# Kernel tuning notes

Measured on AMD Instinct MI355X. Metric: run time of the kernel, lower is better.

Reference implementation:

```python
import jax, jax.numpy as jnp
import numpy as np

NEVENT = 1024
NSTEP = 64
NWINDOW = 2048
NHID = 128
NLAYER = 2


def _lstm_layer(x, Wih, Whh, bih, bhh):
    # x: [B, T, D]; PyTorch gate order: i, f, g, o
    B = x.shape[0]
    H = Whh.shape[1]
    h0 = jnp.zeros((B, H), x.dtype)
    c0 = jnp.zeros((B, H), x.dtype)
    b = bih + bhh

    def step(carry, xt):
        h, c = carry
        gates = xt @ Wih.T + h @ Whh.T + b  # [B, 4H]
        i, f, g, o = jnp.split(gates, 4, axis=-1)
        i = jax.nn.sigmoid(i)
        f = jax.nn.sigmoid(f)
        g = jnp.tanh(g)
        o = jax.nn.sigmoid(o)
        c = f * c + i * g
        h = o * jnp.tanh(c)
        return (h, c), h

    _, ys = jax.lax.scan(step, (h0, c0), jnp.swapaxes(x, 0, 1))  # ys: [T, B, H]
    return jnp.swapaxes(ys, 0, 1)


def _lstm(x, layers):
    for p in layers:
        x = _lstm_layer(x, *p)
    return x


def setup_inputs() -> dict:
    key = jax.random.key(0)
    ks = jax.random.split(key, 32)
    bound = 1.0 / np.sqrt(NHID)

    def u(k, shape):
        return jax.random.uniform(k, shape, jnp.float32, -bound, bound)

    inp = {"sequential": jax.random.randint(ks[0], (NWINDOW, NSTEP), 0, NEVENT)}
    i = 1
    for name, in0 in [("seq", 1), ("quant", NEVENT)]:
        for l in range(NLAYER):
            d = in0 if l == 0 else NHID
            inp[f"{name}_Wih{l}"] = u(ks[i], (4 * NHID, d)); i += 1
            inp[f"{name}_Whh{l}"] = u(ks[i], (4 * NHID, NHID)); i += 1
            inp[f"{name}_bih{l}"] = u(ks[i], (4 * NHID,)); i += 1
            inp[f"{name}_bhh{l}"] = u(ks[i], (4 * NHID,)); i += 1
    inp["cls_W"] = u(ks[i], (NEVENT, 2 * NHID)); i += 1
    inp["cls_b"] = u(ks[i], (NEVENT,))
    return inp


def reference(sequential,
              seq_Wih0, seq_Whh0, seq_bih0, seq_bhh0,
              seq_Wih1, seq_Whh1, seq_bih1, seq_bhh1,
              quant_Wih0, quant_Whh0, quant_bih0, quant_bhh0,
              quant_Wih1, quant_Whh1, quant_bih1, quant_bhh1,
              cls_W, cls_b):
    # sequential branch: embed (nemb=1 -> unsqueeze) then 2-layer LSTM
    seq_x = sequential[:, :, None].astype(jnp.float32)  # [B, T, 1]
    seq_out = _lstm(seq_x, [(seq_Wih0, seq_Whh0, seq_bih0, seq_bhh0),
                            (seq_Wih1, seq_Whh1, seq_bih1, seq_bhh1)])

    # quantitative branch: cumulative event-count histogram per window
    # (vectorized equivalent of the nested Counter loops): one-hot + cumsum over time
    quant = jnp.cumsum(jax.nn.one_hot(sequential, NEVENT, dtype=jnp.float32), axis=1)  # [B, T, E]
    quant_out = _lstm(quant, [(quant_Wih0, quant_Whh0, quant_bih0, quant_bhh0),
                              (quant_Wih1, quant_Whh1, quant_bih1, quant_bhh1)])

    out = jnp.concatenate([seq_out[:, -1], quant_out[:, -1]], axis=1)  # [B, 2H]
    return out @ cls_W.T + cls_b  # [B, nevent]
```

## Files before the change

kernel.cpp:

```cpp
#include <hip/hip_runtime.h>
#include <hip/hip_bf16.h>
#include <math.h>

#define NEVENT 1024
#define NSTEP 64
#define NWINDOW 2048
#define NHID 128
#define NG 512
#define WPB 8

typedef __attribute__((ext_vector_type(8))) short bf16x8;
typedef __attribute__((ext_vector_type(4))) float f32x4;

__device__ __forceinline__ unsigned short f2bf(float f){
  unsigned int u = __float_as_uint(f);
  return (unsigned short)((u + 0x7FFFu + ((u >> 16) & 1u)) >> 16);
}
__device__ __forceinline__ float sigm(float x){
  return __builtin_amdgcn_rcpf(1.0f + __expf(-x));
}
__device__ __forceinline__ float tanh_f(float x){
  float e = __expf(2.0f * x);
  return 1.0f - 2.0f * __builtin_amdgcn_rcpf(e + 1.0f);
}
__device__ __forceinline__ void lgkm_barrier(){
  asm volatile("s_waitcnt lgkmcnt(0)" ::: "memory");
  __builtin_amdgcn_s_barrier();
}
#define SWZ(row, byte) ((byte) ^ (((row) & 7) << 4))

__global__ void transpose_k(const float* __restrict__ in, float* __restrict__ out, int R, int C){
  int idx = blockIdx.x*256 + threadIdx.x;
  if (idx < R*C){ int r = idx / C, c = idx - r*C; out[c*R + r] = in[idx]; }
}

__global__ void pack6_k(const float* __restrict__ s0, const float* __restrict__ s1,
                        const float* __restrict__ s2, const float* __restrict__ s3,
                        const float* __restrict__ s4, const float* __restrict__ s5,
                        unsigned short* __restrict__ dst){
  int g = blockIdx.x >> 5;
  int i = (blockIdx.x & 31)*256 + threadIdx.x;
  const float* src = (g==0)?s0:(g==1)?s1:(g==2)?s2:(g==3)?s3:(g==4)?s4:s5;
  unsigned short* d = dst + g*65536;
  int lane = i & 63; int n = (i >> 6) & 31; int kt = i >> 11;
  int col = 16*n + (lane & 15);
  int k0  = 32*kt + 8*(lane >> 4);
  #pragma unroll
  for (int j = 0; j < 8; ++j)
    d[i*8 + j] = f2bf(src[col*128 + k0 + j]);
}

__global__ __launch_bounds__(512, 2)
void lstm_fused_k(const int* __restrict__ seqtok,
    const float* __restrict__ sWih0,
    const float* __restrict__ sb0i, const float* __restrict__ sb0h,
    const float* __restrict__ sb1i, const float* __restrict__ sb1h,
    const float* __restrict__ qb0i, const float* __restrict__ qb0h,
    const float* __restrict__ qb1i, const float* __restrict__ qb1h,
    const unsigned short* __restrict__ pWhh0_s, const unsigned short* __restrict__ pWih1_s,
    const unsigned short* __restrict__ pWhh1_s,
    const unsigned short* __restrict__ pWhh0_q, const unsigned short* __restrict__ pWih1_q,
    const unsigned short* __restrict__ pWhh1_q,
    const float* __restrict__ qWqT,
    float* __restrict__ hseq, float* __restrict__ hq)
{
  __shared__ uint4 wih1[8192];
  __shared__ __attribute__((aligned(16))) unsigned short h0buf[2][2048];
  __shared__ __attribute__((aligned(16))) unsigned short h1buf[2][2048];
  __shared__ int sAll[16*64];

  const int tid  = threadIdx.x;
  const int lane = tid & 63;
  const int nw   = tid >> 6;
  const bool quant = (blockIdx.x >= 128);
  const int blk  = quant ? (int)blockIdx.x - 128 : (int)blockIdx.x;
  const int w0   = blk * 16;

  const uint4* wsrc = (const uint4*)(quant ? pWih1_q : pWih1_s);
  for (int i = tid; i < 8192; i += 512) wih1[i] = wsrc[i];
  for (int i = tid; i < 16*64; i += 512){ int w = i >> 6, t = i & 63; sAll[i] = seqtok[(w0 + w)*64 + t]; }
  for (int i = tid; i < 2048; i += 512){ h0buf[0][i] = 0; h1buf[0][i] = 0; }

  const int jcol  = 16*nw + (lane & 15);
  const int rbase = 4*(lane >> 4);
  const float* b0i = quant ? qb0i : sb0i; const float* b0h = quant ? qb0h : sb0h;
  const float* b1i = quant ? qb1i : sb1i; const float* b1h = quant ? qb1h : sb1h;
  float b0c[4], b1c[4], wc[4];
  #pragma unroll
  for (int q = 0; q < 4; ++q){
    int col = 128*q + jcol;
    b0c[q] = b0i[col] + b0h[col];
    b1c[q] = b1i[col] + b1h[col];
    wc[q]  = sWih0[col];
  }

  const unsigned short* p0 = quant ? pWhh0_q : pWhh0_s;
  const unsigned short* p1 = quant ? pWhh1_q : pWhh1_s;
  bf16x8 whh0f[4][4], whh1f[4][4];
  #pragma unroll
  for (int q = 0; q < 4; ++q)
    #pragma unroll
    for (int kt = 0; kt < 4; ++kt){
      int idx = ((kt*32 + 8*q + nw)*64 + lane)*8;
      whh0f[q][kt] = *(const bf16x8*)(p0 + idx);
      whh1f[q][kt] = *(const bf16x8*)(p1 + idx);
    }

  float zr[4][4], pref[4][4];
  float c0[4] = {0,0,0,0}, c1[4] = {0,0,0,0};
  #pragma unroll
  for (int q = 0; q < 4; ++q)
    #pragma unroll
    for (int r = 0; r < 4; ++r){ zr[q][r] = b0c[q]; pref[q][r] = 0.0f; }

  char* const h0base = (char*)h0buf;
  char* const h1base = (char*)h1buf;
  float* const houtp = quant ? hq : hseq;

  __syncthreads();

  {
    float g0[4][4];
    if (quant){
      #pragma unroll
      for (int r = 0; r < 4; ++r){
        int s = sAll[(rbase + r)*64 + 0];
        #pragma unroll
        for (int q = 0; q < 4; ++q) pref[q][r] = qWqT[s*512 + 128*q + jcol];
      }
      #pragma unroll
      for (int q = 0; q < 4; ++q)
        #pragma unroll
        for (int r = 0; r < 4; ++r){ zr[q][r] += pref[q][r]; g0[q][r] = zr[q][r]; }
      #pragma unroll
      for (int r = 0; r < 4; ++r){
        int s = sAll[(rbase + r)*64 + 1];
        #pragma unroll
        for (int q = 0; q < 4; ++q) pref[q][r] = qWqT[s*512 + 128*q + jcol];
      }
    } else {
      #pragma unroll
      for (int r = 0; r < 4; ++r){
        float sv = (float)sAll[(rbase + r)*64 + 0];
        #pragma unroll
        for (int q = 0; q < 4; ++q) g0[q][r] = fmaf(sv, wc[q], b0c[q]);
      }
    }
    #pragma unroll
    for (int r = 0; r < 4; ++r){
      float iv = sigm(g0[0][r]);
      float gv = tanh_f(g0[2][r]);
      float ov = sigm(g0[3][r]);
      c0[r] = iv * gv;
      float h = ov * tanh_f(c0[r]);
      int row = rbase + r;
      *(unsigned short*)(h0base + 4096 + SWZ(row, row*256 + jcol*2)) = f2bf(h);
    }
  }
  __syncthreads();

  for (int t = 0; t < NSTEP-1; ++t){
    char* h0rd = h0base + ((t+1)&1)*4096;
    char* h1rd = h1base + ((t  )&1)*4096;
    char* h0wr = h0base + ((t  )&1)*4096;
    char* h1wr = h1base + ((t+1)&1)*4096;

    {
      f32x4 acc[4];
      #pragma unroll
      for (int q = 0; q < 4; ++q){ f32x4 a; a[0]=b1c[q]; a[1]=b1c[q]; a[2]=b1c[q]; a[3]=b1c[q]; acc[q] = a; }
      #pragma unroll
      for (int kt = 0; kt < 4; ++kt){
        int row = lane & 15;
        int off = SWZ(row, row*256 + kt*64 + (lane>>4)*16);
        const bf16x8 a0 = *(const bf16x8*)(h0rd + off);
        const bf16x8 a1 = *(const bf16x8*)(h1rd + off);
        #pragma unroll
        for (int q = 0; q < 4; ++q){
          const bf16x8 wi = *(const bf16x8*)((const char*)wih1 + ((kt*32 + 8*q + nw)*64 + lane)*16);
          acc[q] = __builtin_amdgcn_mfma_f32_16x16x32_bf16(a0, wi,           acc[q], 0, 0, 0);
          acc[q] = __builtin_amdgcn_mfma_f32_16x16x32_bf16(a1, whh1f[q][kt], acc[q], 0, 0, 0);
        }
      }
      #pragma unroll
      for (int r = 0; r < 4; ++r){
        float iv = sigm(acc[0][r]), fv = sigm(acc[1][r]);
        float gv = tanh_f(acc[2][r]), ov = sigm(acc[3][r]);
        c1[r] = fv*c1[r] + iv*gv;
        float h = ov * tanh_f(c1[r]);
        int row = rbase + r;
        *(unsigned short*)(h1wr + SWZ(row, row*256 + jcol*2)) = f2bf(h);
      }
    }

    {
      f32x4 acc[4];
      if (quant){
        #pragma unroll
        for (int q = 0; q < 4; ++q){
          f32x4 a;
          #pragma unroll
          for (int r = 0; r < 4; ++r){ zr[q][r] += pref[q][r]; a[r] = zr[q][r]; }
          acc[q] = a;
        }
        if (t < NSTEP-2){
          #pragma unroll
          for (int r = 0; r < 4; ++r){
            int s = sAll[(rbase + r)*64 + t + 2];
            #pragma unroll
            for (int q = 0; q < 4; ++q) pref[q][r] = qWqT[s*512 + 128*q + jcol];
          }
        }
      } else {
        float sv[4];
        #pragma unroll
        for (int r = 0; r < 4; ++r) sv[r] = (float)sAll[(rbase + r)*64 + t + 1];
        #pragma unroll
        for (int q = 0; q < 4; ++q){
          f32x4 a;
          #pragma unroll
          for (int r = 0; r < 4; ++r) a[r] = fmaf(sv[r], wc[q], b0c[q]);
          acc[q] = a;
        }
      }
      #pragma unroll
      for (int kt = 0; kt < 4; ++kt){
        int row = lane & 15;
        int off = SWZ(row, row*256 + kt*64 + (lane>>4)*16);
        const bf16x8 a0 = *(const bf16x8*)(h0rd + off);
        #pragma unroll
        for (int q = 0; q < 4; ++q)
          acc[q] = __builtin_amdgcn_mfma_f32_16x16x32_bf16(a0, whh0f[q][kt], acc[q], 0, 0, 0);
      }
      #pragma unroll
      for (int r = 0; r < 4; ++r){
        float iv = sigm(acc[0][r]), fv = sigm(acc[1][r]);
        float gv = tanh_f(acc[2][r]), ov = sigm(acc[3][r]);
        c0[r] = fv*c0[r] + iv*gv;
        float h = ov * tanh_f(c0[r]);
        int row = rbase + r;
        *(unsigned short*)(h0wr + SWZ(row, row*256 + jcol*2)) = f2bf(h);
      }
    }

    lgkm_barrier();
  }

  {
    const int t = NSTEP-1;
    char* h0rd = h0base + ((t+1)&1)*4096;
    char* h1rd = h1base + ((t  )&1)*4096;
    f32x4 acc[4];
    #pragma unroll
    for (int q = 0; q < 4; ++q){ f32x4 a; a[0]=b1c[q]; a[1]=b1c[q]; a[2]=b1c[q]; a[3]=b1c[q]; acc[q] = a; }
    #pragma unroll
    for (int kt = 0; kt < 4; ++kt){
      int row = lane & 15;
      int off = SWZ(row, row*256 + kt*64 + (lane>>4)*16);
      const bf16x8 a0 = *(const bf16x8*)(h0rd + off);
      const bf16x8 a1 = *(const bf16x8*)(h1rd + off);
      #pragma unroll
      for (int q = 0; q < 4; ++q){
        const bf16x8 wi = *(const bf16x8*)((const char*)wih1 + ((kt*32 + 8*q + nw)*64 + lane)*16);
        acc[q] = __builtin_amdgcn_mfma_f32_16x16x32_bf16(a0, wi,           acc[q], 0, 0, 0);
        acc[q] = __builtin_amdgcn_mfma_f32_16x16x32_bf16(a1, whh1f[q][kt], acc[q], 0, 0, 0);
      }
    }
    #pragma unroll
    for (int r = 0; r < 4; ++r){
      float iv = sigm(acc[0][r]), fv = sigm(acc[1][r]);
      float gv = tanh_f(acc[2][r]), ov = sigm(acc[3][r]);
      c1[r] = fv*c1[r] + iv*gv;
      float h = ov * tanh_f(c1[r]);
      int row = rbase + r;
      houtp[(w0 + row)*128 + jcol] = h;
    }
  }
}

__global__ __launch_bounds__(256, 4)
void cls_k(const float* __restrict__ hseq, const float* __restrict__ hq,
           const float* __restrict__ clsWT, const float* __restrict__ clsb,
           float* __restrict__ out)
{
  __shared__ float hcat[WPB][2*NHID];
  const int tid = threadIdx.x;
  const int w0 = blockIdx.x * WPB;
  for (int i = tid; i < WPB*2*NHID; i += 256){
    int w = i >> 8; int j = i & (2*NHID-1);
    hcat[w][j] = (j < NHID) ? hseq[(w0+w)*NHID + j] : hq[(w0+w)*NHID + (j - NHID)];
  }
  __syncthreads();
  float acc[4][WPB];
  #pragma unroll
  for (int p=0;p<4;++p)
    #pragma unroll
    for (int w=0;w<WPB;++w) acc[p][w] = 0.0f;
  for (int j = 0; j < 2*NHID; ++j){
    float wv0 = clsWT[j*NEVENT + tid];
    float wv1 = clsWT[j*NEVENT + tid + 256];
    float wv2 = clsWT[j*NEVENT + tid + 512];
    float wv3 = clsWT[j*NEVENT + tid + 768];
    #pragma unroll
    for (int w=0; w<WPB; ++w){
      float hv = hcat[w][j];
      acc[0][w] = fmaf(hv, wv0, acc[0][w]);
      acc[1][w] = fmaf(hv, wv1, acc[1][w]);
      acc[2][w] = fmaf(hv, wv2, acc[2][w]);
      acc[3][w] = fmaf(hv, wv3, acc[3][w]);
    }
  }
  #pragma unroll
  for (int p=0;p<4;++p){
    float bb = clsb[tid + p*256];
    #pragma unroll
    for (int w=0;w<WPB;++w)
      out[(w0+w)*NEVENT + tid + p*256] = acc[p][w] + bb;
  }
}

extern "C" void kernel_launch(void* const* d_in, const int* in_sizes, int n_in,
                              void* d_out, int out_size, void* d_ws, size_t ws_size,
                              hipStream_t stream) {
  const int*   seqtok = (const int*)  d_in[0];
  const float* sWih0  = (const float*)d_in[1];
  const float* sWhh0  = (const float*)d_in[2];
  const float* sb0i   = (const float*)d_in[3];
  const float* sb0h   = (const float*)d_in[4];
  const float* sWih1  = (const float*)d_in[5];
  const float* sWhh1  = (const float*)d_in[6];
  const float* sb1i   = (const float*)d_in[7];
  const float* sb1h   = (const float*)d_in[8];
  const float* qWih0  = (const float*)d_in[9];
  const float* qWhh0  = (const float*)d_in[10];
  const float* qb0i   = (const float*)d_in[11];
  const float* qb0h   = (const float*)d_in[12];
  const float* qWih1  = (const float*)d_in[13];
  const float* qWhh1  = (const float*)d_in[14];
  const float* qb1i   = (const float*)d_in[15];
  const float* qb1h   = (const float*)d_in[16];
  const float* clsW   = (const float*)d_in[17];
  const float* clsb   = (const float*)d_in[18];

  float* ws = (float*)d_ws;
  float* qWqT  = ws;
  float* clsWT = ws + 524288;
  float* hseq  = ws + 786432;
  float* hq    = ws + 1048576;
  unsigned short* pk = (unsigned short*)(ws + 1310720);
  unsigned short* pWhh0_s = pk;
  unsigned short* pWih1_s = pk + 65536;
  unsigned short* pWhh1_s = pk + 131072;
  unsigned short* pWhh0_q = pk + 196608;
  unsigned short* pWih1_q = pk + 262144;
  unsigned short* pWhh1_q = pk + 327680;

  transpose_k<<<(NG*NEVENT + 255)/256, 256, 0, stream>>>(qWih0, qWqT, NG, NEVENT);
  transpose_k<<<(NEVENT*2*NHID + 255)/256, 256, 0, stream>>>(clsW, clsWT, NEVENT, 2*NHID);
  pack6_k<<<192, 256, 0, stream>>>(sWhh0, sWih1, sWhh1, qWhh0, qWih1, qWhh1, pk);

  lstm_fused_k<<<256, 512, 0, stream>>>(seqtok, sWih0,
      sb0i, sb0h, sb1i, sb1h, qb0i, qb0h, qb1i, qb1h,
      pWhh0_s, pWih1_s, pWhh1_s, pWhh0_q, pWih1_q, pWhh1_q,
      qWqT, hseq, hq);

  cls_k<<<NWINDOW/WPB, 256, 0, stream>>>(hseq, hq, clsWT, clsb, (float*)d_out);
}
```

Baseline: 224.5 us.

## Fuse prep kernels with tiled transpose and hold Wih1 fragments in registers

Merges the two transpose launches and the pack kernel into one prep kernel, and replaces the naive strided transpose with a 32x32 shared-memory tiled transpose so both reads and writes are coalesced. In the LSTM kernel, the layer-1 input weights move from a 128KB shared-memory array into per-thread register fragments, which removes their LDS reads each step and frees LDS. The layer-0 step also reuses the h0 fragments already loaded for layer 1 instead of reading them from LDS again. The cost is 64 more VGPRs per thread for the extra fragments, under launch bounds of 512 threads and 2 blocks, so register spills or lower occupancy are possible.

Measured after the change: 485.5 us. 2.16x slower.

```diff
diff --git a/kernel.cpp b/kernel.cpp
--- a/kernel.cpp
+++ b/kernel.cpp
@@ -29,25 +29,47 @@
 }
 #define SWZ(row, byte) ((byte) ^ (((row) & 7) << 4))
 
-__global__ void transpose_k(const float* __restrict__ in, float* __restrict__ out, int R, int C){
-  int idx = blockIdx.x*256 + threadIdx.x;
-  if (idx < R*C){ int r = idx / C, c = idx - r*C; out[c*R + r] = in[idx]; }
-}
-
-__global__ void pack6_k(const float* __restrict__ s0, const float* __restrict__ s1,
-                        const float* __restrict__ s2, const float* __restrict__ s3,
-                        const float* __restrict__ s4, const float* __restrict__ s5,
-                        unsigned short* __restrict__ dst){
-  int g = blockIdx.x >> 5;
-  int i = (blockIdx.x & 31)*256 + threadIdx.x;
-  const float* src = (g==0)?s0:(g==1)?s1:(g==2)?s2:(g==3)?s3:(g==4)?s4:s5;
-  unsigned short* d = dst + g*65536;
-  int lane = i & 63; int n = (i >> 6) & 31; int kt = i >> 11;
-  int col = 16*n + (lane & 15);
-  int k0  = 32*kt + 8*(lane >> 4);
-  #pragma unroll
-  for (int j = 0; j < 8; ++j)
-    d[i*8 + j] = f2bf(src[col*128 + k0 + j]);
+__global__ __launch_bounds__(256)
+void prep_k(const float* __restrict__ qWih0, float* __restrict__ qWqT,
+            const float* __restrict__ clsW,  float* __restrict__ clsWT,
+            const float* __restrict__ s0, const float* __restrict__ s1,
+            const float* __restrict__ s2, const float* __restrict__ s3,
+            const float* __restrict__ s4, const float* __restrict__ s5,
+            unsigned short* __restrict__ dst)
+{
+  const int b = blockIdx.x;
+  if (b < 768){
+    const float* in; float* out; int R, C, bb;
+    if (b < 512){ in = qWih0; out = qWqT; R = NG;     C = NEVENT; bb = b; }
+    else        { in = clsW;  out = clsWT; R = NEVENT; C = 2*NHID; bb = b - 512; }
+    __shared__ float tl[32][33];
+    const int nbx = C >> 5;
+    const int by = bb / nbx, bx = bb - by*nbx;
+    const int tx = threadIdx.x & 31, ty = threadIdx.x >> 5;
+    #pragma unroll
+    for (int k = 0; k < 4; ++k){
+      int r = by*32 + ty + k*8;
+      tl[ty + k*8][tx] = in[r*C + bx*32 + tx];
+    }
+    __syncthreads();
+    #pragma unroll
+    for (int k = 0; k < 4; ++k){
+      int r = bx*32 + ty + k*8;
+      out[r*R + by*32 + tx] = tl[tx][ty + k*8];
+    }
+  } else {
+    const int bb = b - 768;
+    const int g = bb >> 5;
+    const int i = (bb & 31)*256 + threadIdx.x;
+    const float* src = (g==0)?s0:(g==1)?s1:(g==2)?s2:(g==3)?s3:(g==4)?s4:s5;
+    unsigned short* d = dst + g*65536;
+    const int lane = i & 63; const int n = (i >> 6) & 31; const int kt = i >> 11;
+    const int col = 16*n + (lane & 15);
+    const int k0  = 32*kt + 8*(lane >> 4);
+    #pragma unroll
+    for (int j = 0; j < 8; ++j)
+      d[i*8 + j] = f2bf(src[col*128 + k0 + j]);
+  }
 }
 
 __global__ __launch_bounds__(512, 2)
@@ -64,7 +86,6 @@
     const float* __restrict__ qWqT,
     float* __restrict__ hseq, float* __restrict__ hq)
 {
-  __shared__ uint4 wih1[8192];
   __shared__ __attribute__((aligned(16))) unsigned short h0buf[2][2048];
   __shared__ __attribute__((aligned(16))) unsigned short h1buf[2][2048];
   __shared__ int sAll[16*64];
@@ -76,8 +97,6 @@
   const int blk  = quant ? (int)blockIdx.x - 128 : (int)blockIdx.x;
   const int w0   = blk * 16;
 
-  const uint4* wsrc = (const uint4*)(quant ? pWih1_q : pWih1_s);
-  for (int i = tid; i < 8192; i += 512) wih1[i] = wsrc[i];
   for (int i = tid; i < 16*64; i += 512){ int w = i >> 6, t = i & 63; sAll[i] = seqtok[(w0 + w)*64 + t]; }
   for (int i = tid; i < 2048; i += 512){ h0buf[0][i] = 0; h1buf[0][i] = 0; }
 
@@ -96,7 +115,8 @@
 
   const unsigned short* p0 = quant ? pWhh0_q : pWhh0_s;
   const unsigned short* p1 = quant ? pWhh1_q : pWhh1_s;
-  bf16x8 whh0f[4][4], whh1f[4][4];
+  const unsigned short* pw = quant ? pWih1_q : pWih1_s;
+  bf16x8 whh0f[4][4], whh1f[4][4], wih1f[4][4];
   #pragma unroll
   for (int q = 0; q < 4; ++q)
     #pragma unroll
@@ -104,6 +124,7 @@
       int idx = ((kt*32 + 8*q + nw)*64 + lane)*8;
       whh0f[q][kt] = *(const bf16x8*)(p0 + idx);
       whh1f[q][kt] = *(const bf16x8*)(p1 + idx);
+      wih1f[q][kt] = *(const bf16x8*)(pw + idx);
     }
 
   float zr[4][4], pref[4][4];
@@ -165,6 +186,8 @@
     char* h0wr = h0base + ((t  )&1)*4096;
     char* h1wr = h1base + ((t+1)&1)*4096;
 
+    bf16x8 a0f[4];
+
     {
       f32x4 acc[4];
       #pragma unroll
@@ -175,10 +198,10 @@
         int off = SWZ(row, row*256 + kt*64 + (lane>>4)*16);
         const bf16x8 a0 = *(const bf16x8*)(h0rd + off);
         const bf16x8 a1 = *(const bf16x8*)(h1rd + off);
+        a0f[kt] = a0;
         #pragma unroll
         for (int q = 0; q < 4; ++q){
-          const bf16x8 wi = *(const bf16x8*)((const char*)wih1 + ((kt*32 + 8*q + nw)*64 + lane)*16);
-          acc[q] = __builtin_amdgcn_mfma_f32_16x16x32_bf16(a0, wi,           acc[q], 0, 0, 0);
+          acc[q] = __builtin_amdgcn_mfma_f32_16x16x32_bf16(a0, wih1f[q][kt], acc[q], 0, 0, 0);
           acc[q] = __builtin_amdgcn_mfma_f32_16x16x32_bf16(a1, whh1f[q][kt], acc[q], 0, 0, 0);
         }
       }
@@ -224,14 +247,10 @@
         }
       }
       #pragma unroll
-      for (int kt = 0; kt < 4; ++kt){
-        int row = lane & 15;
-        int off = SWZ(row, row*256 + kt*64 + (lane>>4)*16);
-        const bf16x8 a0 = *(const bf16x8*)(h0rd + off);
+      for (int kt = 0; kt < 4; ++kt)
         #pragma unroll
         for (int q = 0; q < 4; ++q)
-          acc[q] = __builtin_amdgcn_mfma_f32_16x16x32_bf16(a0, whh0f[q][kt], acc[q], 0, 0, 0);
-      }
+          acc[q] = __builtin_amdgcn_mfma_f32_16x16x32_bf16(a0f[kt], whh0f[q][kt], acc[q], 0, 0, 0);
       #pragma unroll
       for (int r = 0; r < 4; ++r){
         float iv = sigm(acc[0][r]), fv = sigm(acc[1][r]);
@@ -261,8 +280,7 @@
       const bf16x8 a1 = *(const bf16x8*)(h1rd + off);
       #pragma unroll
       for (int q = 0; q < 4; ++q){
-        const bf16x8 wi = *(const bf16x8*)((const char*)wih1 + ((kt*32 + 8*q + nw)*64 + lane)*16);
-        acc[q] = __builtin_amdgcn_mfma_f32_16x16x32_bf16(a0, wi,           acc[q], 0, 0, 0);
+        acc[q] = __builtin_amdgcn_mfma_f32_16x16x32_bf16(a0, wih1f[q][kt], acc[q], 0, 0, 0);
         acc[q] = __builtin_amdgcn_mfma_f32_16x16x32_bf16(a1, whh1f[q][kt], acc[q], 0, 0, 0);
       }
     }
@@ -355,9 +373,8 @@
   unsigned short* pWih1_q = pk + 262144;
   unsigned short* pWhh1_q = pk + 327680;
 
-  transpose_k<<<(NG*NEVENT + 255)/256, 256, 0, stream>>>(qWih0, qWqT, NG, NEVENT);
-  transpose_k<<<(NEVENT*2*NHID + 255)/256, 256, 0, stream>>>(clsW, clsWT, NEVENT, 2*NHID);
-  pack6_k<<<192, 256, 0, stream>>>(sWhh0, sWih1, sWhh1, qWhh0, qWih1, qWhh1, pk);
+  prep_k<<<960, 256, 0, stream>>>(qWih0, qWqT, clsW, clsWT,
+      sWhh0, sWih1, sWhh1, qWhh0, qWih1, qWhh1, pk);
 
   lstm_fused_k<<<256, 512, 0, stream>>>(seqtok, sWih0,
       sb0i, sb0h, sb1i, sb1h, qb0i, qb0h, qb1i, qb1h,
```
